# Optimization experiments

Hardware: AMD Instinct MI355X
Metric: run time of the kernel (lower is better)

## Reference

```python
import jax, jax.numpy as jnp
import numpy as np

N = 50000      # nodes
E = 400000     # edges (before self-loops)
IN = 128       # input feature dim
HID = 32       # out_channels per head
HEADS = 12
NC = 2         # num_classes
SLOPE = 0.2    # GATv2 leaky_relu negative slope


def setup_inputs() -> dict:
    key = jax.random.key(0)
    ks = jax.random.split(key, 24)
    f32 = jnp.float32
    def nrm(k, shape, s=0.1):
        return jax.random.normal(k, shape, dtype=f32) * s
    inp = {}
    inp["x"] = jax.random.normal(ks[0], (N, IN), dtype=f32)
    inp["edge_index"] = jax.random.randint(ks[1], (2, E), 0, N, dtype=jnp.int32)
    # GATv2 layer 0: in=IN, layer 1: in=HID; both heads=HEADS, out=HID, concat=False
    dims = [IN, HID]
    i = 2
    for l, d in enumerate(dims):
        inp[f"Wl{l}"] = nrm(ks[i], (d, HEADS * HID)); i += 1
        inp[f"bl{l}"] = jnp.zeros((HEADS * HID,), f32)
        inp[f"Wr{l}"] = nrm(ks[i], (d, HEADS * HID)); i += 1
        inp[f"br{l}"] = jnp.zeros((HEADS * HID,), f32)
        inp[f"att{l}"] = nrm(ks[i], (HEADS, HID)); i += 1
        inp[f"bias{l}"] = jnp.zeros((HID,), f32)
    # output GATv2Conv(HID, NC): heads=1, concat=True
    inp["Wlo"] = nrm(ks[i], (HID, NC)); i += 1
    inp["blo"] = jnp.zeros((NC,), f32)
    inp["Wro"] = nrm(ks[i], (HID, NC)); i += 1
    inp["bro"] = jnp.zeros((NC,), f32)
    inp["atto"] = nrm(ks[i], (1, NC)); i += 1
    inp["biaso"] = jnp.zeros((NC,), f32)
    return inp


def gatv2_conv(x, src, dst, Wl, bl, Wr, br, att, bias, heads, out_ch, concat):
    """PyG GATv2Conv (share_weights=False, self-loops pre-appended, eval mode)."""
    n = x.shape[0]
    xl = (x @ Wl + bl).reshape(n, heads, out_ch)   # source transform
    xr = (x @ Wr + br).reshape(n, heads, out_ch)   # target transform
    # per-edge attention: e_ij = att . leaky_relu(xl_j + xr_i)
    h = jax.nn.leaky_relu(xl[src] + xr[dst], SLOPE)            # [E, H, C]
    logits = jnp.einsum('ehc,hc->eh', h, att)                   # [E, H]
    # segment softmax over incoming edges per destination node
    m = jax.ops.segment_max(logits, dst, num_segments=n)        # [N, H]
    a = jnp.exp(logits - m[dst])
    denom = jax.ops.segment_sum(a, dst, num_segments=n)         # [N, H]
    alpha = a / (denom[dst] + 1e-16)                            # [E, H]
    out = jax.ops.segment_sum(xl[src] * alpha[..., None], dst, num_segments=n)
    out = out.reshape(n, heads * out_ch) if concat else out.mean(axis=1)
    return out + bias


def reference(x, edge_index, Wl0, bl0, Wr0, br0, att0, bias0,
              Wl1, bl1, Wr1, br1, att1, bias1,
              Wlo, blo, Wro, bro, atto, biaso):
    n = x.shape[0]
    loop = jnp.arange(n, dtype=edge_index.dtype)
    src = jnp.concatenate([edge_index[0], loop])  # add self-loops (PyG default)
    dst = jnp.concatenate([edge_index[1], loop])
    h = gatv2_conv(x, src, dst, Wl0, bl0, Wr0, br0, att0, bias0, HEADS, HID, False)
    h = jax.nn.elu(h)
    h = gatv2_conv(h, src, dst, Wl1, bl1, Wr1, br1, att1, bias1, HEADS, HID, False)
    h = jax.nn.elu(h)
    out = gatv2_conv(h, src, dst, Wlo, blo, Wro, bro, atto, biaso, 1, NC, True)
    return out
```

## Files before the change

kernel.cpp:

```cpp
#include <hip/hip_runtime.h>
#include <hip/hip_fp16.h>
#include <math.h>

#define IN_DIM 128
#define HID 32
#define HEADS 12
#define FDIM (HEADS*HID)
#define SLOPE 0.2f

typedef __attribute__((ext_vector_type(8))) short short8;
typedef __attribute__((ext_vector_type(4))) float float4v;
typedef __attribute__((ext_vector_type(4))) float f32x4;
typedef _Float16 hv2 __attribute__((ext_vector_type(2)));

__device__ __forceinline__ float dot2acc(hv2 a, hv2 b, float c) {
#if __has_builtin(__builtin_amdgcn_fdot2)
    return __builtin_amdgcn_fdot2(a, b, c, false);
#else
    return c + (float)a.x * (float)b.x + (float)a.y * (float)b.y;
#endif
}

__device__ __forceinline__ void async_cp16(const void* g, void* l) {
    __builtin_amdgcn_global_load_lds(
        (const __attribute__((address_space(1))) void*)g,
        (__attribute__((address_space(3))) void*)l, 16, 0, 0);
}


__global__ void hist_kernel(const int* __restrict__ dst, int* __restrict__ cnt, int E) {
    int e = blockIdx.x * blockDim.x + threadIdx.x;
    if (e < E) atomicAdd(&cnt[dst[e]], 1);
}

__global__ __launch_bounds__(256) void scan_partial_kernel(const int* __restrict__ cnt,
                                                           int* __restrict__ partials, int n) {
    int i = blockIdx.x * 256 + threadIdx.x;
    int v = (i < n) ? cnt[i] : 0;
#pragma unroll
    for (int off = 1; off < 64; off <<= 1) v += __shfl_xor(v, off);
    __shared__ int sh[4];
    if ((threadIdx.x & 63) == 0) sh[threadIdx.x >> 6] = v;
    __syncthreads();
    if (threadIdx.x == 0) partials[blockIdx.x] = sh[0] + sh[1] + sh[2] + sh[3];
}

__global__ __launch_bounds__(1024) void scan_top_kernel(int* __restrict__ partials, int nb) {
    __shared__ int sh[1024];
    int t = threadIdx.x;
    int v = (t < nb) ? partials[t] : 0;
    sh[t] = v;
    __syncthreads();
    for (int off = 1; off < 1024; off <<= 1) {
        int u = (t >= off) ? sh[t - off] : 0;
        __syncthreads();
        sh[t] += u;
        __syncthreads();
    }
    if (t < nb) partials[t] = sh[t] - v;
}

__global__ __launch_bounds__(256) void scan_final_kernel(const int* __restrict__ cnt,
                                                         const int* __restrict__ partials,
                                                         int* __restrict__ start,
                                                         int* __restrict__ cursor, int n) {
    __shared__ int sh[256];
    int t = threadIdx.x;
    int i = blockIdx.x * 256 + t;
    int v = (i < n) ? cnt[i] : 0;
    sh[t] = v;
    __syncthreads();
    for (int off = 1; off < 256; off <<= 1) {
        int u = (t >= off) ? sh[t - off] : 0;
        __syncthreads();
        sh[t] += u;
        __syncthreads();
    }
    int ex = sh[t] - v + partials[blockIdx.x];
    if (i < n) {
        start[i] = ex;
        cursor[i] = ex;
        if (i == n - 1) start[n] = ex + v;
    }
}

__global__ void scatter_kernel(const int* __restrict__ src, const int* __restrict__ dst,
                               int* __restrict__ cursor, int* __restrict__ srcs,
                               int* __restrict__ srcsOff, int E) {
    int e = blockIdx.x * blockDim.x + threadIdx.x;
    if (e < E) {
        int d = dst[e];
        int pos = atomicAdd(&cursor[d], 1);
        int s = src[e];
        srcs[pos] = s;
        srcsOff[pos] = s * (FDIM * 2);
    }
}


__device__ __forceinline__ unsigned int bf16_rne(float f) {
    unsigned int u = __float_as_uint(f);
    return (u + 0x7FFFu + ((u >> 16) & 1u)) >> 16;
}


__global__ void prep_all(const float* __restrict__ Wl0, const float* __restrict__ Wr0,
                         const float* __restrict__ Wl1, const float* __restrict__ Wr1,
                         const float* __restrict__ a0, const float* __restrict__ a1,
                         short* __restrict__ Bl0h, short* __restrict__ Bl0l,
                         short* __restrict__ Br0h, short* __restrict__ Br0l,
                         short* __restrict__ Bl1h, short* __restrict__ Bl1l,
                         short* __restrict__ Br1h, short* __restrict__ Br1l,
                         _Float16* __restrict__ attH) {
    int idx = blockIdx.x * 256 + threadIdx.x;
    if (idx < 49152) {
        int k = idx / 384, n = idx - k * 384;
        float w1 = Wl0[idx], w2 = Wr0[idx];
        unsigned int h1 = bf16_rne(w1);
        unsigned int l1 = bf16_rne(w1 - __uint_as_float(h1 << 16));
        unsigned int h2 = bf16_rne(w2);
        unsigned int l2 = bf16_rne(w2 - __uint_as_float(h2 << 16));
        Bl0h[n * 128 + k] = (short)h1;  Bl0l[n * 128 + k] = (short)l1;
        Br0h[n * 128 + k] = (short)h2;  Br0l[n * 128 + k] = (short)l2;
    } else if (idx < 61440) {
        int i2 = idx - 49152;
        int k = i2 / 384, n = i2 - k * 384;
        float w1 = Wl1[i2], w2 = Wr1[i2];
        unsigned int h1 = bf16_rne(w1);
        unsigned int l1 = bf16_rne(w1 - __uint_as_float(h1 << 16));
        unsigned int h2 = bf16_rne(w2);
        unsigned int l2 = bf16_rne(w2 - __uint_as_float(h2 << 16));
        Bl1h[n * 32 + k] = (short)h1;  Bl1l[n * 32 + k] = (short)l1;
        Br1h[n * 32 + k] = (short)h2;  Br1l[n * 32 + k] = (short)l2;
    } else if (idx < 62208) {
        int i2 = idx - 61440;
        attH[i2] = (_Float16)((i2 < 384) ? a0[i2] : a1[i2 - 384]);
    }
}


__global__ void conv_x_kernel(const float* __restrict__ A, short* __restrict__ Ah,
                              short* __restrict__ Al, int total4) {
    int i = blockIdx.x * 256 + threadIdx.x;
    if (i >= total4) return;
    float4 v = ((const float4*)A)[i];
    float fs[4] = {v.x, v.y, v.z, v.w};
    unsigned int hb[4], lb[4];
#pragma unroll
    for (int t = 0; t < 4; t++) {
        hb[t] = bf16_rne(fs[t]);
        lb[t] = bf16_rne(fs[t] - __uint_as_float(hb[t] << 16));
    }
    uint2 hp, lp;
    hp.x = hb[0] | (hb[1] << 16); hp.y = hb[2] | (hb[3] << 16);
    lp.x = lb[0] | (lb[1] << 16); lp.y = lb[2] | (lb[3] << 16);
    ((uint2*)Ah)[i] = hp;
    ((uint2*)Al)[i] = lp;
}


__global__ __launch_bounds__(256) void gemm_pair_async(
    const short* __restrict__ Ahi, const short* __restrict__ Alo,
    const short* __restrict__ B1h, const short* __restrict__ B1l,
    const float* __restrict__ bias1, __half* __restrict__ C1,
    const short* __restrict__ B2h, const short* __restrict__ B2l,
    const float* __restrict__ bias2, __half* __restrict__ C2,
    int M, int K) {
    __shared__ __align__(16) unsigned char smem[33792];
    int tid = threadIdx.x;
    int lane = tid & 63;
    int wave = tid >> 6;
    int wm = wave & 1, wn = wave >> 1;
    int rowBase = blockIdx.x * 128;
    bool second = blockIdx.y >= 3;
    int colBase = (blockIdx.y - (second ? 3 : 0)) * 128;
    const short* Bh  = second ? B2h : B1h;
    const short* Bl  = second ? B2l : B1l;
    const float* bias = second ? bias2 : bias1;
    __half*      C    = second ? C2 : C1;

    const short8* AsHi = (const short8*)smem;
    const short8* AsLo = (const short8*)(smem + 8192);
    const short8* BsHi = (const short8*)(smem + 16384);
    const short8* BsLo = (const short8*)(smem + 24576);

    const short* gsrc[8];
    void* ldst[8];
#pragma unroll
    for (int q = 0; q < 8; q++) {
        int t  = (q & 1) * 4 + wave;
        int rc = t * 16 + (lane & 15);
        int ko = (lane >> 4) * 8;
        const short* base = (q < 2) ? Ahi : (q < 4) ? Alo : (q < 6) ? Bh : Bl;
        int rb = (q < 4) ? rowBase : colBase;
        gsrc[q] = base + (long)(rb + rc) * K + ko;
        ldst[q] = (void*)(smem + q * 4096 + wave * 1024);
    }

    float4v acc[4][4];
#pragma unroll
    for (int i = 0; i < 4; i++)
#pragma unroll
        for (int j = 0; j < 4; j++) acc[i][j] = (float4v){0.f, 0.f, 0.f, 0.f};

    for (int kt = 0; kt < K; kt += 32) {
#pragma unroll
        for (int q = 0; q < 8; q++) {
            async_cp16(gsrc[q], ldst[q]);
            gsrc[q] += 32;
        }
        __syncthreads();

        short8 ah[4], al[4], bh[4], blv[4];
#pragma unroll
        for (int i = 0; i < 4; i++) {
            ah[i]  = AsHi[(wm * 4 + i) * 64 + lane];
            al[i]  = AsLo[(wm * 4 + i) * 64 + lane];
            bh[i]  = BsHi[(wn * 4 + i) * 64 + lane];
            blv[i] = BsLo[(wn * 4 + i) * 64 + lane];
        }
#pragma unroll
        for (int i = 0; i < 4; i++)
#pragma unroll
            for (int j = 0; j < 4; j++) {
                acc[i][j] = __builtin_amdgcn_mfma_f32_16x16x32_bf16(ah[i], bh[j],  acc[i][j], 0, 0, 0);
                acc[i][j] = __builtin_amdgcn_mfma_f32_16x16x32_bf16(ah[i], blv[j], acc[i][j], 0, 0, 0);
                acc[i][j] = __builtin_amdgcn_mfma_f32_16x16x32_bf16(al[i], bh[j],  acc[i][j], 0, 0, 0);
            }
        __syncthreads();
    }

    float* Ct = (float*)smem;
    int cq = lane >> 4, cn = lane & 15;
#pragma unroll
    for (int ph = 0; ph < 2; ph++) {
        if (wm == ph) {
#pragma unroll
            for (int i = 0; i < 4; i++)
#pragma unroll
                for (int j = 0; j < 4; j++) {
                    int lr = i * 16 + cq * 4;
                    int lc = wn * 64 + j * 16 + cn;
#pragma unroll
                    for (int r = 0; r < 4; r++)
                        Ct[(lr + r) * 132 + lc] = acc[i][j][r];
                }
        }
        __syncthreads();
#pragma unroll
        for (int k = 0; k < 4; k++) {
            int o = k * 256 + tid;
            int lr = o >> 4;
            int oc = (o & 15) << 3;
            int gr = rowBase + ph * 64 + lr;
            if (gr < M) {
                float4 f0 = *(float4*)&Ct[lr * 132 + oc];
                float4 f1 = *(float4*)&Ct[lr * 132 + oc + 4];
                int gc = colBase + oc;
                float4 b0 = *(const float4*)(bias + gc);
                float4 b1 = *(const float4*)(bias + gc + 4);
                __half2 p0 = __floats2half2_rn(f0.x + b0.x, f0.y + b0.y);
                __half2 p1 = __floats2half2_rn(f0.z + b0.z, f0.w + b0.w);
                __half2 p2 = __floats2half2_rn(f1.x + b1.x, f1.y + b1.y);
                __half2 p3 = __floats2half2_rn(f1.z + b1.z, f1.w + b1.w);
                uint4 ov;
                ov.x = *(unsigned int*)&p0;
                ov.y = *(unsigned int*)&p1;
                ov.z = *(unsigned int*)&p2;
                ov.w = *(unsigned int*)&p3;
                *(uint4*)(C + (size_t)gr * FDIM + gc) = ov;
            }
        }
        __syncthreads();
    }
}


__global__ __launch_bounds__(64) void agg_kernel(const __half* __restrict__ xl,
                                                 const __half* __restrict__ xr,
                                                 const _Float16* __restrict__ att_h,
                                                 const float* __restrict__ bias,
                                                 const int* __restrict__ start,
                                                 const int* __restrict__ srcsOff,
                                                 short* __restrict__ houtHi,
                                                 short* __restrict__ houtLo,
                                                 const float* __restrict__ Wl,
                                                 const float* __restrict__ bl,
                                                 const float* __restrict__ Wr,
                                                 const float* __restrict__ br,
                                                 float* __restrict__ xloB,
                                                 float* __restrict__ xroB, int N) {
    int node = blockIdx.x;
    if (node >= N) return;
    int lane = threadIdx.x & 63;
    int hl = lane & 31;
    int half_ = lane >> 5;
    int cb = hl << 3;

    long nodeOff = (long)node * (FDIM * 2);
    hv2 xr2[6], at2[6];
    f32x4 acc[3];
    float s[3];
#pragma unroll
    for (int c = 0; c < 3; c++) {
        uint2 ur = *(const uint2*)((const char*)xr + nodeOff + c * 256 + cb);
        xr2[2*c]   = __builtin_bit_cast(hv2, ur.x);
        xr2[2*c+1] = __builtin_bit_cast(hv2, ur.y);
        uint2 ua = *(const uint2*)((const char*)att_h + c * 256 + cb);
        at2[2*c]   = __builtin_bit_cast(hv2, ua.x);
        at2[2*c+1] = __builtin_bit_cast(hv2, ua.y);
        acc[c] = (f32x4){0.f, 0.f, 0.f, 0.f};
        s[c] = 0.f;
    }
    const hv2 sl2 = {(_Float16)SLOPE, (_Float16)SLOPE};
    const char* xlb = (const char*)xl;

    int e0 = start[node], e1 = start[node + 1];

    for (int b = e0 - 1; b < e1; b += 4) {
        hv2 xa[2][6];
        float mask[2];
#pragma unroll
        for (int p = 0; p < 2; p++) {
            int myIdx = b + p * 2 + half_;
            int ic = min(myIdx, e1 - 1);
            long off = (ic < e0) ? nodeOff : (long)srcsOff[ic];
            mask[p] = (myIdx < e1) ? 0.f : -1e30f;
            const char* base = xlb + off + cb;
            uint2 u0 = *(const uint2*)(base);
            uint2 u1 = *(const uint2*)(base + 256);
            uint2 u2 = *(const uint2*)(base + 512);
            xa[p][0] = __builtin_bit_cast(hv2, u0.x); xa[p][1] = __builtin_bit_cast(hv2, u0.y);
            xa[p][2] = __builtin_bit_cast(hv2, u1.x); xa[p][3] = __builtin_bit_cast(hv2, u1.y);
            xa[p][4] = __builtin_bit_cast(hv2, u2.x); xa[p][5] = __builtin_bit_cast(hv2, u2.y);
        }
#pragma unroll
        for (int p = 0; p < 2; p++) {
            float pc[3];
#pragma unroll
            for (int c = 0; c < 3; c++) {
                hv2 t0 = xa[p][2*c]   + xr2[2*c];
                hv2 t1 = xa[p][2*c+1] + xr2[2*c+1];
                t0 = __builtin_elementwise_max(t0, t0 * sl2);
                t1 = __builtin_elementwise_max(t1, t1 * sl2);
                pc[c] = dot2acc(t1, at2[2*c+1], dot2acc(t0, at2[2*c], 0.f));
            }
#pragma unroll
            for (int st = 1; st <= 4; st <<= 1) {
                pc[0] += __shfl_xor(pc[0], st);
                pc[1] += __shfl_xor(pc[1], st);
                pc[2] += __shfl_xor(pc[2], st);
            }
#pragma unroll
            for (int c = 0; c < 3; c++) {
                float a = __expf(pc[c] + mask[p]);
                s[c] += a;
                acc[c].x = fmaf(a, (float)xa[p][2*c].x,   acc[c].x);
                acc[c].y = fmaf(a, (float)xa[p][2*c].y,   acc[c].y);
                acc[c].z = fmaf(a, (float)xa[p][2*c+1].x, acc[c].z);
                acc[c].w = fmaf(a, (float)xa[p][2*c+1].y, acc[c].w);
            }
        }
    }

#pragma unroll
    for (int c = 0; c < 3; c++) {
        acc[c].x += __shfl_xor(acc[c].x, 32);
        acc[c].y += __shfl_xor(acc[c].y, 32);
        acc[c].z += __shfl_xor(acc[c].z, 32);
        acc[c].w += __shfl_xor(acc[c].w, 32);
        s[c] += __shfl_xor(s[c], 32);
    }
    f32x4 v[3];
#pragma unroll
    for (int c = 0; c < 3; c++) {
        float inv = 1.f / (s[c] + 1e-16f);
        f32x4 iv = {inv, inv, inv, inv};
        v[c] = acc[c] * iv;
    }
#pragma unroll
    for (int st = 8; st <= 16; st <<= 1) {
#pragma unroll
        for (int c = 0; c < 3; c++) {
            v[c].x += __shfl_xor(v[c].x, st);
            v[c].y += __shfl_xor(v[c].y, st);
            v[c].z += __shfl_xor(v[c].z, st);
            v[c].w += __shfl_xor(v[c].w, st);
        }
    }
    if (lane < 8) {
        f32x4 b4 = *(const f32x4*)(bias + (hl << 2));
        f32x4 o = (v[0] + v[1] + v[2]) * (f32x4){1.f/12.f, 1.f/12.f, 1.f/12.f, 1.f/12.f} + b4;
        o.x = o.x > 0.f ? o.x : expm1f(o.x);
        o.y = o.y > 0.f ? o.y : expm1f(o.y);
        o.z = o.z > 0.f ? o.z : expm1f(o.z);
        o.w = o.w > 0.f ? o.w : expm1f(o.w);
        if (houtHi) {
            float fs[4] = {o.x, o.y, o.z, o.w};
            unsigned int hb[4], lb[4];
#pragma unroll
            for (int t = 0; t < 4; t++) {
                hb[t] = bf16_rne(fs[t]);
                lb[t] = bf16_rne(fs[t] - __uint_as_float(hb[t] << 16));
            }
            uint2 hp, lp;
            hp.x = hb[0] | (hb[1] << 16); hp.y = hb[2] | (hb[3] << 16);
            lp.x = lb[0] | (lb[1] << 16); lp.y = lb[2] | (lb[3] << 16);
            *(uint2*)(houtHi + (size_t)node * 32 + (hl << 2)) = hp;
            *(uint2*)(houtLo + (size_t)node * 32 + (hl << 2)) = lp;
        }
        if (Wl) {
            f32x4 wl0 = *(const f32x4*)(Wl + (hl << 3));
            f32x4 wl1 = *(const f32x4*)(Wl + (hl << 3) + 4);
            f32x4 wr0 = *(const f32x4*)(Wr + (hl << 3));
            f32x4 wr1 = *(const f32x4*)(Wr + (hl << 3) + 4);
            float l0 = o.x * wl0.x + o.y * wl0.z + o.z * wl1.x + o.w * wl1.z;
            float l1 = o.x * wl0.y + o.y * wl0.w + o.z * wl1.y + o.w * wl1.w;
            float r0 = o.x * wr0.x + o.y * wr0.z + o.z * wr1.x + o.w * wr1.z;
            float r1 = o.x * wr0.y + o.y * wr0.w + o.z * wr1.y + o.w * wr1.w;
#pragma unroll
            for (int st = 1; st <= 4; st <<= 1) {
                l0 += __shfl_xor(l0, st); l1 += __shfl_xor(l1, st);
                r0 += __shfl_xor(r0, st); r1 += __shfl_xor(r1, st);
            }
            if (hl == 0) {
                xloB[2 * node]     = l0 + bl[0];
                xloB[2 * node + 1] = l1 + bl[1];
                xroB[2 * node]     = r0 + br[0];
                xroB[2 * node + 1] = r1 + br[1];
            }
        }
    }
}


__global__ __launch_bounds__(256) void out_agg_kernel(const float* __restrict__ xlo,
                                                      const float* __restrict__ xro,
                                                      const float* __restrict__ atto,
                                                      const float* __restrict__ biaso,
                                                      const int* __restrict__ start,
                                                      const int* __restrict__ srcs,
                                                      float* __restrict__ out, int N) {
    int g = (blockIdx.x * blockDim.x + threadIdx.x) >> 3;
    int j = threadIdx.x & 7;
    if (g >= N) return;
    float a0 = atto[0], a1 = atto[1];
    float xr0 = xro[2 * g], xr1 = xro[2 * g + 1];
    float s = 0.f, acc0 = 0.f, acc1 = 0.f;
    int e0 = start[g], e1 = start[g + 1];
    for (int idx = e0 - 1 + j; idx < e1; idx += 8) {
        int jj = (idx < e0) ? g : srcs[idx];
        float x0 = xlo[2 * jj], x1 = xlo[2 * jj + 1];
        float t0 = x0 + xr0, t1 = x1 + xr1;
        t0 = fmaxf(t0, SLOPE * t0);
        t1 = fmaxf(t1, SLOPE * t1);
        float L = a0 * t0 + a1 * t1;
        float a = __expf(L);
        s += a;
        acc0 = fmaf(a, x0, acc0);
        acc1 = fmaf(a, x1, acc1);
    }
#pragma unroll
    for (int st = 1; st <= 4; st <<= 1) {
        s    += __shfl_xor(s, st);
        acc0 += __shfl_xor(acc0, st);
        acc1 += __shfl_xor(acc1, st);
    }
    if (j == 0) {
        float inv = 1.0f / (s + 1e-16f);
        out[2 * g]     = acc0 * inv + biaso[0];
        out[2 * g + 1] = acc1 * inv + biaso[1];
    }
}


extern "C" void kernel_launch(void* const* d_in, const int* in_sizes, int n_in,
                              void* d_out, int out_size, void* d_ws, size_t ws_size,
                              hipStream_t stream) {
    const float* x    = (const float*)d_in[0];
    const int*   ei   = (const int*)d_in[1];
    const float* Wl0  = (const float*)d_in[2];
    const float* bl0  = (const float*)d_in[3];
    const float* Wr0  = (const float*)d_in[4];
    const float* br0  = (const float*)d_in[5];
    const float* att0 = (const float*)d_in[6];
    const float* bias0= (const float*)d_in[7];
    const float* Wl1  = (const float*)d_in[8];
    const float* bl1  = (const float*)d_in[9];
    const float* Wr1  = (const float*)d_in[10];
    const float* br1  = (const float*)d_in[11];
    const float* att1 = (const float*)d_in[12];
    const float* bias1= (const float*)d_in[13];
    const float* Wlo  = (const float*)d_in[14];
    const float* blo  = (const float*)d_in[15];
    const float* Wro  = (const float*)d_in[16];
    const float* bro  = (const float*)d_in[17];
    const float* atto = (const float*)d_in[18];
    const float* biaso= (const float*)d_in[19];

    const int N = in_sizes[0] / IN_DIM;
    const int E = in_sizes[1] / 2;

    char* ws = (char*)d_ws;
    size_t off = 0;
    auto take = [&](size_t bytes) -> char* {
        char* p = ws + off;
        off += (bytes + 255) & ~(size_t)255;
        return p;
    };
    __half* xlf = (__half*)take((size_t)N * FDIM * 2);
    __half* xrf = (__half*)take((size_t)N * FDIM * 2);
    float* xloB = (float*)take((size_t)N * 2 * 4);
    float* xroB = (float*)take((size_t)N * 2 * 4);
    int* cnt    = (int*)take((size_t)N * 4);
    int* startA = (int*)take((size_t)(N + 1) * 4);
    int* cursor = (int*)take((size_t)N * 4);
    int* srcs   = (int*)take((size_t)E * 4);
    int* srcsOff= (int*)take((size_t)E * 4);
    int  nb     = (N + 255) / 256;
    int* partials = (int*)take((size_t)nb * 4);
    short* Bl0h = (short*)take((size_t)FDIM * IN_DIM * 2);
    short* Bl0l = (short*)take((size_t)FDIM * IN_DIM * 2);
    short* Br0h = (short*)take((size_t)FDIM * IN_DIM * 2);
    short* Br0l = (short*)take((size_t)FDIM * IN_DIM * 2);
    short* Bl1h = (short*)take((size_t)FDIM * HID * 2);
    short* Bl1l = (short*)take((size_t)FDIM * HID * 2);
    short* Br1h = (short*)take((size_t)FDIM * HID * 2);
    short* Br1l = (short*)take((size_t)FDIM * HID * 2);
    short* xh   = (short*)take((size_t)N * IN_DIM * 2);
    short* xlo_ = (short*)take((size_t)N * IN_DIM * 2);
    short* h0h  = (short*)take((size_t)N * HID * 2);
    short* h0l  = (short*)take((size_t)N * HID * 2);
    _Float16* attH = (_Float16*)take((size_t)768 * 2);
    (void)take(32768);

    const int* esrc = ei;
    const int* edst = ei + E;

    prep_all<<<(62208 + 255) / 256, 256, 0, stream>>>(Wl0, Wr0, Wl1, Wr1, att0, att1,
                                                      Bl0h, Bl0l, Br0h, Br0l,
                                                      Bl1h, Bl1l, Br1h, Br1l, attH);
    conv_x_kernel<<<((N * IN_DIM / 4) + 255) / 256, 256, 0, stream>>>(x, xh, xlo_, N * IN_DIM / 4);

    hipMemsetAsync(cnt, 0, (size_t)N * 4, stream);
    hist_kernel<<<(E + 255) / 256, 256, 0, stream>>>(edst, cnt, E);
    scan_partial_kernel<<<nb, 256, 0, stream>>>(cnt, partials, N);
    scan_top_kernel<<<1, 1024, 0, stream>>>(partials, nb);
    scan_final_kernel<<<nb, 256, 0, stream>>>(cnt, partials, startA, cursor, N);
    scatter_kernel<<<(E + 255) / 256, 256, 0, stream>>>(esrc, edst, cursor, srcs, srcsOff, E);

    dim3 ggrid((N + 127) / 128, 6);
    gemm_pair_async<<<ggrid, 256, 0, stream>>>(xh, xlo_, Bl0h, Bl0l, bl0, xlf, Br0h, Br0l, br0, xrf, N, IN_DIM);
    agg_kernel<<<N, 64, 0, stream>>>(xlf, xrf, attH, bias0, startA, srcsOff,
                                     h0h, h0l, nullptr, nullptr, nullptr, nullptr,
                                     nullptr, nullptr, N);
    gemm_pair_async<<<ggrid, 256, 0, stream>>>(h0h, h0l, Bl1h, Bl1l, bl1, xlf, Br1h, Br1l, br1, xrf, N, HID);
    agg_kernel<<<N, 64, 0, stream>>>(xlf, xrf, attH + 384, bias1, startA, srcsOff,
                                     nullptr, nullptr, Wlo, blo, Wro, bro,
                                     xloB, xroB, N);
    out_agg_kernel<<<((size_t)N * 8 + 255) / 256, 256, 0, stream>>>(xloB, xroB, atto, biaso, startA, srcs, (float*)d_out, N);
}
```

Baseline: 382.5 us.

## Remap GATv2 aggregation so each lane owns one head of one edge

The aggregation kernel changes its work split. Before, 32 lanes covered one edge's 384 features and used shuffle reductions for the per-head dot products. Now each of 60 lanes handles one head (32 channels) of one of 5 edges at a time, so the attention logit is computed within a lane with no shuffles. Partial sums are combined across the 5 edge slots through a per-wave LDS buffer with a rotated layout to avoid bank conflicts. Blocks now hold 4 waves, each processing its own node. The trade-off is far more registers per lane (16 accumulator vectors plus xr/att copies), which may lower occupancy, and 4 lanes per wave sit idle.

```diff
diff --git a/kernel.cpp b/kernel.cpp
--- a/kernel.cpp
+++ b/kernel.cpp
@@ -276,159 +276,158 @@
 }
 
 
-__global__ __launch_bounds__(64) void agg_kernel(const __half* __restrict__ xl,
-                                                 const __half* __restrict__ xr,
-                                                 const _Float16* __restrict__ att_h,
-                                                 const float* __restrict__ bias,
-                                                 const int* __restrict__ start,
-                                                 const int* __restrict__ srcsOff,
-                                                 short* __restrict__ houtHi,
-                                                 short* __restrict__ houtLo,
-                                                 const float* __restrict__ Wl,
-                                                 const float* __restrict__ bl,
-                                                 const float* __restrict__ Wr,
-                                                 const float* __restrict__ br,
-                                                 float* __restrict__ xloB,
-                                                 float* __restrict__ xroB, int N) {
-    int node = blockIdx.x;
+__global__ __launch_bounds__(256) void agg_kernel(const __half* __restrict__ xl,
+                                                  const __half* __restrict__ xr,
+                                                  const _Float16* __restrict__ att_h,
+                                                  const float* __restrict__ bias,
+                                                  const int* __restrict__ start,
+                                                  const int* __restrict__ srcsOff,
+                                                  short* __restrict__ houtHi,
+                                                  short* __restrict__ houtLo,
+                                                  const float* __restrict__ Wl,
+                                                  const float* __restrict__ bl,
+                                                  const float* __restrict__ Wr,
+                                                  const float* __restrict__ br,
+                                                  float* __restrict__ xloB,
+                                                  float* __restrict__ xroB, int N) {
+    __shared__ float lds[4][2048];
+    int wave = threadIdx.x >> 6;
+    int lane = threadIdx.x & 63;
+    int node = blockIdx.x * 4 + wave;
     if (node >= N) return;
-    int lane = threadIdx.x & 63;
-    int hl = lane & 31;
-    int half_ = lane >> 5;
-    int cb = hl << 3;
+    float* W = lds[wave];
+
+    int h = lane % 12;
+    int slot = (lane < 60) ? (lane / 12) : (1 << 28);
 
     long nodeOff = (long)node * (FDIM * 2);
-    hv2 xr2[6], at2[6];
-    f32x4 acc[3];
-    float s[3];
-#pragma unroll
-    for (int c = 0; c < 3; c++) {
-        uint2 ur = *(const uint2*)((const char*)xr + nodeOff + c * 256 + cb);
-        xr2[2*c]   = __builtin_bit_cast(hv2, ur.x);
-        xr2[2*c+1] = __builtin_bit_cast(hv2, ur.y);
-        uint2 ua = *(const uint2*)((const char*)att_h + c * 256 + cb);
-        at2[2*c]   = __builtin_bit_cast(hv2, ua.x);
-        at2[2*c+1] = __builtin_bit_cast(hv2, ua.y);
-        acc[c] = (f32x4){0.f, 0.f, 0.f, 0.f};
-        s[c] = 0.f;
+    int hb = h << 6;
+
+    hv2 xr2[16], at2[16];
+    {
+        const uint4* xrp = (const uint4*)((const char*)xr + nodeOff + hb);
+        const uint4* atp = (const uint4*)((const char*)att_h + hb);
+#pragma unroll
+        for (int q = 0; q < 4; q++) {
+            uint4 u = xrp[q];
+            xr2[q * 4 + 0] = __builtin_bit_cast(hv2, u.x);
+            xr2[q * 4 + 1] = __builtin_bit_cast(hv2, u.y);
+            xr2[q * 4 + 2] = __builtin_bit_cast(hv2, u.z);
+            xr2[q * 4 + 3] = __builtin_bit_cast(hv2, u.w);
+            uint4 v = atp[q];
+            at2[q * 4 + 0] = __builtin_bit_cast(hv2, v.x);
+            at2[q * 4 + 1] = __builtin_bit_cast(hv2, v.y);
+            at2[q * 4 + 2] = __builtin_bit_cast(hv2, v.z);
+            at2[q * 4 + 3] = __builtin_bit_cast(hv2, v.w);
+        }
     }
     const hv2 sl2 = {(_Float16)SLOPE, (_Float16)SLOPE};
     const char* xlb = (const char*)xl;
 
     int e0 = start[node], e1 = start[node + 1];
 
-    for (int b = e0 - 1; b < e1; b += 4) {
-        hv2 xa[2][6];
-        float mask[2];
-#pragma unroll
-        for (int p = 0; p < 2; p++) {
-            int myIdx = b + p * 2 + half_;
-            int ic = min(myIdx, e1 - 1);
-            long off = (ic < e0) ? nodeOff : (long)srcsOff[ic];
-            mask[p] = (myIdx < e1) ? 0.f : -1e30f;
-            const char* base = xlb + off + cb;
-            uint2 u0 = *(const uint2*)(base);
-            uint2 u1 = *(const uint2*)(base + 256);
-            uint2 u2 = *(const uint2*)(base + 512);
-            xa[p][0] = __builtin_bit_cast(hv2, u0.x); xa[p][1] = __builtin_bit_cast(hv2, u0.y);
-            xa[p][2] = __builtin_bit_cast(hv2, u1.x); xa[p][3] = __builtin_bit_cast(hv2, u1.y);
-            xa[p][4] = __builtin_bit_cast(hv2, u2.x); xa[p][5] = __builtin_bit_cast(hv2, u2.y);
-        }
-#pragma unroll
-        for (int p = 0; p < 2; p++) {
-            float pc[3];
-#pragma unroll
-            for (int c = 0; c < 3; c++) {
-                hv2 t0 = xa[p][2*c]   + xr2[2*c];
-                hv2 t1 = xa[p][2*c+1] + xr2[2*c+1];
-                t0 = __builtin_elementwise_max(t0, t0 * sl2);
-                t1 = __builtin_elementwise_max(t1, t1 * sl2);
-                pc[c] = dot2acc(t1, at2[2*c+1], dot2acc(t0, at2[2*c], 0.f));
+    float s = 0.f;
+    f32x4 acc[8];
+#pragma unroll
+    for (int q = 0; q < 8; q++) acc[q] = (f32x4){0.f, 0.f, 0.f, 0.f};
+
+    for (int base = e0 - 1; base < e1; base += 5) {
+        int myIdx = base + slot;
+        int ic = min(myIdx, e1 - 1);
+        long off = (ic < e0) ? nodeOff : (long)srcsOff[ic];
+        float mask = (myIdx < e1) ? 0.f : -1e30f;
+        const uint4* p = (const uint4*)(xlb + off + hb);
+        uint4 u0 = p[0], u1 = p[1], u2 = p[2], u3 = p[3];
+        hv2 xa[16];
+        xa[0]  = __builtin_bit_cast(hv2, u0.x); xa[1]  = __builtin_bit_cast(hv2, u0.y);
+        xa[2]  = __builtin_bit_cast(hv2, u0.z); xa[3]  = __builtin_bit_cast(hv2, u0.w);
+        xa[4]  = __builtin_bit_cast(hv2, u1.x); xa[5]  = __builtin_bit_cast(hv2, u1.y);
+        xa[6]  = __builtin_bit_cast(hv2, u1.z); xa[7]  = __builtin_bit_cast(hv2, u1.w);
+        xa[8]  = __builtin_bit_cast(hv2, u2.x); xa[9]  = __builtin_bit_cast(hv2, u2.y);
+        xa[10] = __builtin_bit_cast(hv2, u2.z); xa[11] = __builtin_bit_cast(hv2, u2.w);
+        xa[12] = __builtin_bit_cast(hv2, u3.x); xa[13] = __builtin_bit_cast(hv2, u3.y);
+        xa[14] = __builtin_bit_cast(hv2, u3.z); xa[15] = __builtin_bit_cast(hv2, u3.w);
+
+        float pc0 = 0.f, pc1 = 0.f;
+#pragma unroll
+        for (int k = 0; k < 16; k += 2) {
+            hv2 t0 = xa[k] + xr2[k];
+            hv2 t1 = xa[k + 1] + xr2[k + 1];
+            t0 = __builtin_elementwise_max(t0, t0 * sl2);
+            t1 = __builtin_elementwise_max(t1, t1 * sl2);
+            pc0 = dot2acc(t0, at2[k], pc0);
+            pc1 = dot2acc(t1, at2[k + 1], pc1);
+        }
+        float a = __expf(pc0 + pc1 + mask);
+        s += a;
+#pragma unroll
+        for (int k = 0; k < 16; k++) {
+            if (k & 1) {
+                acc[k >> 1].z = fmaf(a, (float)xa[k].x, acc[k >> 1].z);
+                acc[k >> 1].w = fmaf(a, (float)xa[k].y, acc[k >> 1].w);
+            } else {
+                acc[k >> 1].x = fmaf(a, (float)xa[k].x, acc[k >> 1].x);
+                acc[k >> 1].y = fmaf(a, (float)xa[k].y, acc[k >> 1].y);
             }
-#pragma unroll
-            for (int st = 1; st <= 4; st <<= 1) {
-                pc[0] += __shfl_xor(pc[0], st);
-                pc[1] += __shfl_xor(pc[1], st);
-                pc[2] += __shfl_xor(pc[2], st);
-            }
-#pragma unroll
-            for (int c = 0; c < 3; c++) {
-                float a = __expf(pc[c] + mask[p]);
-                s[c] += a;
-                acc[c].x = fmaf(a, (float)xa[p][2*c].x,   acc[c].x);
-                acc[c].y = fmaf(a, (float)xa[p][2*c].y,   acc[c].y);
-                acc[c].z = fmaf(a, (float)xa[p][2*c+1].x, acc[c].z);
-                acc[c].w = fmaf(a, (float)xa[p][2*c+1].y, acc[c].w);
-            }
-        }
-    }
-
-#pragma unroll
-    for (int c = 0; c < 3; c++) {
-        acc[c].x += __shfl_xor(acc[c].x, 32);
-        acc[c].y += __shfl_xor(acc[c].y, 32);
-        acc[c].z += __shfl_xor(acc[c].z, 32);
-        acc[c].w += __shfl_xor(acc[c].w, 32);
-        s[c] += __shfl_xor(s[c], 32);
-    }
-    f32x4 v[3];
-#pragma unroll
-    for (int c = 0; c < 3; c++) {
-        float inv = 1.f / (s[c] + 1e-16f);
-        f32x4 iv = {inv, inv, inv, inv};
-        v[c] = acc[c] * iv;
-    }
-#pragma unroll
-    for (int st = 8; st <= 16; st <<= 1) {
-#pragma unroll
-        for (int c = 0; c < 3; c++) {
-            v[c].x += __shfl_xor(v[c].x, st);
-            v[c].y += __shfl_xor(v[c].y, st);
-            v[c].z += __shfl_xor(v[c].z, st);
-            v[c].w += __shfl_xor(v[c].w, st);
-        }
-    }
-    if (lane < 8) {
-        f32x4 b4 = *(const f32x4*)(bias + (hl << 2));
-        f32x4 o = (v[0] + v[1] + v[2]) * (f32x4){1.f/12.f, 1.f/12.f, 1.f/12.f, 1.f/12.f} + b4;
-        o.x = o.x > 0.f ? o.x : expm1f(o.x);
-        o.y = o.y > 0.f ? o.y : expm1f(o.y);
-        o.z = o.z > 0.f ? o.z : expm1f(o.z);
-        o.w = o.w > 0.f ? o.w : expm1f(o.w);
-        if (houtHi) {
-            float fs[4] = {o.x, o.y, o.z, o.w};
-            unsigned int hb[4], lb[4];
-#pragma unroll
-            for (int t = 0; t < 4; t++) {
-                hb[t] = bf16_rne(fs[t]);
-                lb[t] = bf16_rne(fs[t] - __uint_as_float(hb[t] << 16));
-            }
-            uint2 hp, lp;
-            hp.x = hb[0] | (hb[1] << 16); hp.y = hb[2] | (hb[3] << 16);
-            lp.x = lb[0] | (lb[1] << 16); lp.y = lb[2] | (lb[3] << 16);
-            *(uint2*)(houtHi + (size_t)node * 32 + (hl << 2)) = hp;
-            *(uint2*)(houtLo + (size_t)node * 32 + (hl << 2)) = lp;
-        }
-        if (Wl) {
-            f32x4 wl0 = *(const f32x4*)(Wl + (hl << 3));
-            f32x4 wl1 = *(const f32x4*)(Wl + (hl << 3) + 4);
-            f32x4 wr0 = *(const f32x4*)(Wr + (hl << 3));
-            f32x4 wr1 = *(const f32x4*)(Wr + (hl << 3) + 4);
-            float l0 = o.x * wl0.x + o.y * wl0.z + o.z * wl1.x + o.w * wl1.z;
-            float l1 = o.x * wl0.y + o.y * wl0.w + o.z * wl1.y + o.w * wl1.w;
-            float r0 = o.x * wr0.x + o.y * wr0.z + o.z * wr1.x + o.w * wr1.z;
-            float r1 = o.x * wr0.y + o.y * wr0.w + o.z * wr1.y + o.w * wr1.w;
-#pragma unroll
-            for (int st = 1; st <= 4; st <<= 1) {
-                l0 += __shfl_xor(l0, st); l1 += __shfl_xor(l1, st);
-                r0 += __shfl_xor(r0, st); r1 += __shfl_xor(r1, st);
-            }
-            if (hl == 0) {
-                xloB[2 * node]     = l0 + bl[0];
-                xloB[2 * node + 1] = l1 + bl[1];
-                xroB[2 * node]     = r0 + br[0];
-                xroB[2 * node + 1] = r1 + br[1];
-            }
+        }
+    }
+
+    if (lane < 60) {
+#pragma unroll
+        for (int q = 0; q < 8; q++)
+            *(f32x4*)&W[lane * 32 + (((q + lane) & 7) << 2)] = acc[q];
+        W[1920 + lane] = s;
+    }
+    asm volatile("s_waitcnt lgkmcnt(0)" ::: "memory");
+    if (lane < 12) {
+        float sv = W[1920 + lane] + W[1932 + lane] + W[1944 + lane] +
+                   W[1956 + lane] + W[1968 + lane];
+        W[1980 + lane] = 1.f / (sv + 1e-16f);
+    }
+    asm volatile("s_waitcnt lgkmcnt(0)" ::: "memory");
+
+    int c = lane & 31;
+    int g = lane >> 5;
+    float o = 0.f;
+#pragma unroll
+    for (int hh = 0; hh < 6; hh++) {
+        int hd = g * 6 + hh;
+        float inv = W[1980 + hd];
+        float t = 0.f;
+#pragma unroll
+        for (int s5 = 0; s5 < 5; s5++) {
+            int r = hd + 12 * s5;
+            t += W[r * 32 + ((((c >> 2) + r) & 7) << 2) + (c & 3)];
+        }
+        o = fmaf(inv, t, o);
+    }
+    o += __shfl_xor(o, 32);
+    o = o * (1.f / 12.f) + bias[c];
+    o = o > 0.f ? o : expm1f(o);
+
+    if (houtHi) {
+        unsigned int hbi = bf16_rne(o);
+        unsigned int lbi = bf16_rne(o - __uint_as_float(hbi << 16));
+        if (lane < 32) {
+            houtHi[(size_t)node * 32 + c] = (short)hbi;
+            houtLo[(size_t)node * 32 + c] = (short)lbi;
+        }
+    }
+    if (Wl) {
+        float2 wl = *(const float2*)(Wl + 2 * c);
+        float2 wr = *(const float2*)(Wr + 2 * c);
+        float l0 = o * wl.x, l1 = o * wl.y;
+        float r0 = o * wr.x, r1 = o * wr.y;
+#pragma unroll
+        for (int st = 1; st <= 16; st <<= 1) {
+            l0 += __shfl_xor(l0, st); l1 += __shfl_xor(l1, st);
+            r0 += __shfl_xor(r0, st); r1 += __shfl_xor(r1, st);
+        }
+        if (lane == 0) {
+            xloB[2 * node]     = l0 + bl[0];
+            xloB[2 * node + 1] = l1 + bl[1];
+            xroB[2 * node]     = r0 + br[0];
+            xroB[2 * node + 1] = r1 + br[1];
         }
     }
 }
@@ -550,13 +549,14 @@
     scatter_kernel<<<(E + 255) / 256, 256, 0, stream>>>(esrc, edst, cursor, srcs, srcsOff, E);
 
     dim3 ggrid((N + 127) / 128, 6);
+    int aggGrid = (N + 3) / 4;
     gemm_pair_async<<<ggrid, 256, 0, stream>>>(xh, xlo_, Bl0h, Bl0l, bl0, xlf, Br0h, Br0l, br0, xrf, N, IN_DIM);
-    agg_kernel<<<N, 64, 0, stream>>>(xlf, xrf, attH, bias0, startA, srcsOff,
-                                     h0h, h0l, nullptr, nullptr, nullptr, nullptr,
-                                     nullptr, nullptr, N);
+    agg_kernel<<<aggGrid, 256, 0, stream>>>(xlf, xrf, attH, bias0, startA, srcsOff,
+                                            h0h, h0l, nullptr, nullptr, nullptr, nullptr,
+                                            nullptr, nullptr, N);
     gemm_pair_async<<<ggrid, 256, 0, stream>>>(h0h, h0l, Bl1h, Bl1l, bl1, xlf, Br1h, Br1l, br1, xrf, N, HID);
-    agg_kernel<<<N, 64, 0, stream>>>(xlf, xrf, attH + 384, bias1, startA, srcsOff,
-                                     nullptr, nullptr, Wlo, blo, Wro, bro,
-                                     xloB, xroB, N);
+    agg_kernel<<<aggGrid, 256, 0, stream>>>(xlf, xrf, attH + 384, bias1, startA, srcsOff,
+                                            nullptr, nullptr, Wlo, blo, Wro, bro,
+                                            xloB, xroB, N);
     out_agg_kernel<<<((size_t)N * 8 + 255) / 256, 256, 0, stream>>>(xloB, xroB, atto, biaso, startA, srcs, (float*)d_out, N);
 }
```

New measurement: 419.0 us. +9.5%, slower.

## Software-pipeline edge gathers in GAT aggregation and pack four nodes per block

Applied to the files above, without the earlier changes.

Restructures the aggregation loop into a double-buffered pipeline: neighbor offsets are prefetched two steps ahead and feature gathers one step ahead of the softmax/accumulate compute, to hide gather latency. Blocks now hold four wavefronts (one node each) with launch bounds of 256 threads and a min-blocks hint, cutting the grid size fourfold. Offsets switch to 32-bit ints. The extra live registers for two gather buffers raise register pressure, and the last step issues loads for out-of-range indices that get clamped.

```diff
diff --git a/kernel.cpp b/kernel.cpp
--- a/kernel.cpp
+++ b/kernel.cpp
@@ -276,34 +276,34 @@
 }
 
 
-__global__ __launch_bounds__(64) void agg_kernel(const __half* __restrict__ xl,
-                                                 const __half* __restrict__ xr,
-                                                 const _Float16* __restrict__ att_h,
-                                                 const float* __restrict__ bias,
-                                                 const int* __restrict__ start,
-                                                 const int* __restrict__ srcsOff,
-                                                 short* __restrict__ houtHi,
-                                                 short* __restrict__ houtLo,
-                                                 const float* __restrict__ Wl,
-                                                 const float* __restrict__ bl,
-                                                 const float* __restrict__ Wr,
-                                                 const float* __restrict__ br,
-                                                 float* __restrict__ xloB,
-                                                 float* __restrict__ xroB, int N) {
-    int node = blockIdx.x;
+__global__ __launch_bounds__(256, 8) void agg_kernel(const __half* __restrict__ xl,
+                                                     const __half* __restrict__ xr,
+                                                     const _Float16* __restrict__ att_h,
+                                                     const float* __restrict__ bias,
+                                                     const int* __restrict__ start,
+                                                     const int* __restrict__ srcsOff,
+                                                     short* __restrict__ houtHi,
+                                                     short* __restrict__ houtLo,
+                                                     const float* __restrict__ Wl,
+                                                     const float* __restrict__ bl,
+                                                     const float* __restrict__ Wr,
+                                                     const float* __restrict__ br,
+                                                     float* __restrict__ xloB,
+                                                     float* __restrict__ xroB, int N) {
+    int lane = threadIdx.x & 63;
+    int node = blockIdx.x * 4 + (threadIdx.x >> 6);
     if (node >= N) return;
-    int lane = threadIdx.x & 63;
     int hl = lane & 31;
     int half_ = lane >> 5;
     int cb = hl << 3;
 
-    long nodeOff = (long)node * (FDIM * 2);
+    int nodeOffI = node * (FDIM * 2);
     hv2 xr2[6], at2[6];
     f32x4 acc[3];
     float s[3];
 #pragma unroll
     for (int c = 0; c < 3; c++) {
-        uint2 ur = *(const uint2*)((const char*)xr + nodeOff + c * 256 + cb);
+        uint2 ur = *(const uint2*)((const char*)xr + nodeOffI + c * 256 + cb);
         xr2[2*c]   = __builtin_bit_cast(hv2, ur.x);
         xr2[2*c+1] = __builtin_bit_cast(hv2, ur.y);
         uint2 ua = *(const uint2*)((const char*)att_h + c * 256 + cb);
@@ -313,29 +313,37 @@
         s[c] = 0.f;
     }
     const hv2 sl2 = {(_Float16)SLOPE, (_Float16)SLOPE};
-    const char* xlb = (const char*)xl;
+    const char* xlb = (const char*)xl + cb;
 
     int e0 = start[node], e1 = start[node + 1];
-
-    for (int b = e0 - 1; b < e1; b += 4) {
-        hv2 xa[2][6];
-        float mask[2];
+    int e1m1 = e1 - 1;
+
+    auto prepOff = [&](int b, int (&off)[2]) {
 #pragma unroll
         for (int p = 0; p < 2; p++) {
             int myIdx = b + p * 2 + half_;
-            int ic = min(myIdx, e1 - 1);
-            long off = (ic < e0) ? nodeOff : (long)srcsOff[ic];
-            mask[p] = (myIdx < e1) ? 0.f : -1e30f;
-            const char* base = xlb + off + cb;
-            uint2 u0 = *(const uint2*)(base);
-            uint2 u1 = *(const uint2*)(base + 256);
-            uint2 u2 = *(const uint2*)(base + 512);
+            int ic = min(myIdx, e1m1);
+            int so = srcsOff[ic];
+            off[p] = (ic < e0) ? nodeOffI : so;
+        }
+    };
+    auto gather = [&](const int (&off)[2], hv2 (&xa)[2][6]) {
+#pragma unroll
+        for (int p = 0; p < 2; p++) {
+            const char* b = xlb + off[p];
+            uint2 u0 = *(const uint2*)(b);
+            uint2 u1 = *(const uint2*)(b + 256);
+            uint2 u2 = *(const uint2*)(b + 512);
             xa[p][0] = __builtin_bit_cast(hv2, u0.x); xa[p][1] = __builtin_bit_cast(hv2, u0.y);
             xa[p][2] = __builtin_bit_cast(hv2, u1.x); xa[p][3] = __builtin_bit_cast(hv2, u1.y);
             xa[p][4] = __builtin_bit_cast(hv2, u2.x); xa[p][5] = __builtin_bit_cast(hv2, u2.y);
         }
+    };
+    auto compute = [&](int b, const hv2 (&xa)[2][6]) {
 #pragma unroll
         for (int p = 0; p < 2; p++) {
+            int myIdx = b + p * 2 + half_;
+            float mask = (myIdx < e1) ? 0.f : -1e30f;
             float pc[3];
 #pragma unroll
             for (int c = 0; c < 3; c++) {
@@ -353,7 +361,7 @@
             }
 #pragma unroll
             for (int c = 0; c < 3; c++) {
-                float a = __expf(pc[c] + mask[p]);
+                float a = __expf(pc[c] + mask);
                 s[c] += a;
                 acc[c].x = fmaf(a, (float)xa[p][2*c].x,   acc[c].x);
                 acc[c].y = fmaf(a, (float)xa[p][2*c].y,   acc[c].y);
@@ -361,6 +369,27 @@
                 acc[c].w = fmaf(a, (float)xa[p][2*c+1].y, acc[c].w);
             }
         }
+    };
+
+    int offA[2], offB[2];
+    hv2 xaA[2][6], xaB[2][6];
+    int base = e0 - 1;
+    prepOff(base, offA);
+    gather(offA, xaA);
+    prepOff(base + 4, offB);
+
+    while (true) {
+        gather(offB, xaB);
+        prepOff(base + 8, offA);
+        compute(base, xaA);
+        base += 4;
+        if (base >= e1) break;
+
+        gather(offA, xaA);
+        prepOff(base + 8, offB);
+        compute(base, xaB);
+        base += 4;
+        if (base >= e1) break;
     }
 
 #pragma unroll
@@ -550,13 +579,14 @@
     scatter_kernel<<<(E + 255) / 256, 256, 0, stream>>>(esrc, edst, cursor, srcs, srcsOff, E);
 
     dim3 ggrid((N + 127) / 128, 6);
+    int aggGrid = (N + 3) / 4;
     gemm_pair_async<<<ggrid, 256, 0, stream>>>(xh, xlo_, Bl0h, Bl0l, bl0, xlf, Br0h, Br0l, br0, xrf, N, IN_DIM);
-    agg_kernel<<<N, 64, 0, stream>>>(xlf, xrf, attH, bias0, startA, srcsOff,
-                                     h0h, h0l, nullptr, nullptr, nullptr, nullptr,
-                                     nullptr, nullptr, N);
+    agg_kernel<<<aggGrid, 256, 0, stream>>>(xlf, xrf, attH, bias0, startA, srcsOff,
+                                            h0h, h0l, nullptr, nullptr, nullptr, nullptr,
+                                            nullptr, nullptr, N);
     gemm_pair_async<<<ggrid, 256, 0, stream>>>(h0h, h0l, Bl1h, Bl1l, bl1, xlf, Br1h, Br1l, br1, xrf, N, HID);
-    agg_kernel<<<N, 64, 0, stream>>>(xlf, xrf, attH + 384, bias1, startA, srcsOff,
-                                     nullptr, nullptr, Wlo, blo, Wro, bro,
-                                     xloB, xroB, N);
+    agg_kernel<<<aggGrid, 256, 0, stream>>>(xlf, xrf, attH + 384, bias1, startA, srcsOff,
+                                            nullptr, nullptr, Wlo, blo, Wro, bro,
+                                            xloB, xroB, N);
     out_agg_kernel<<<((size_t)N * 8 + 255) / 256, 256, 0, stream>>>(xloB, xroB, atto, biaso, startA, srcs, (float*)d_out, N);
 }
```

Result: slower. 738.3 us (+93.0%).

## Store self-loops in CSR, split mask-free main loop, fold log2e into attention

Applied to the files above, without the earlier changes.

Self-loop edges are now written into the CSR edge list by a new kernel, so the aggregation loops no longer need a per-edge branch for the implicit self edge. The main aggregation loop handles full groups of four edges without masking, and a separate masked tail handles the remainder. Attention vectors are pre-scaled by log2(e) so the softmax can use the hardware exp2 directly, and inline v_fma_mix instructions fuse the fp16-to-fp32 conversion into the accumulate FMAs. This adds one small launch, N extra CSR entries, and some code duplication.

```diff
diff --git a/kernel.cpp b/kernel.cpp
--- a/kernel.cpp
+++ b/kernel.cpp
@@ -7,6 +7,7 @@
 #define HEADS 12
 #define FDIM (HEADS*HID)
 #define SLOPE 0.2f
+#define LOG2E 1.44269504f
 
 typedef __attribute__((ext_vector_type(8))) short short8;
 typedef __attribute__((ext_vector_type(4))) float float4v;
@@ -21,6 +22,27 @@
 #endif
 }
 
+__device__ __forceinline__ float exp2h(float x) {
+#if __has_builtin(__builtin_amdgcn_exp2f)
+    return __builtin_amdgcn_exp2f(x);
+#else
+    return exp2f(x);
+#endif
+}
+
+__device__ __forceinline__ float fma_mix_lo(hv2 x, float a, float c) {
+    float d;
+    asm("v_fma_mix_f32 %0, %1, %2, %3 op_sel_hi:[1,0,0]"
+        : "=v"(d) : "v"(x), "v"(a), "v"(c));
+    return d;
+}
+__device__ __forceinline__ float fma_mix_hi(hv2 x, float a, float c) {
+    float d;
+    asm("v_fma_mix_f32 %0, %1, %2, %3 op_sel:[1,0,0] op_sel_hi:[1,0,0]"
+        : "=v"(d) : "v"(x), "v"(a), "v"(c));
+    return d;
+}
+
 __device__ __forceinline__ void async_cp16(const void* g, void* l) {
     __builtin_amdgcn_global_load_lds(
         (const __attribute__((address_space(1))) void*)g,
@@ -36,7 +58,7 @@
 __global__ __launch_bounds__(256) void scan_partial_kernel(const int* __restrict__ cnt,
                                                            int* __restrict__ partials, int n) {
     int i = blockIdx.x * 256 + threadIdx.x;
-    int v = (i < n) ? cnt[i] : 0;
+    int v = (i < n) ? cnt[i] + 1 : 0;
 #pragma unroll
     for (int off = 1; off < 64; off <<= 1) v += __shfl_xor(v, off);
     __shared__ int sh[4];
@@ -67,7 +89,7 @@
     __shared__ int sh[256];
     int t = threadIdx.x;
     int i = blockIdx.x * 256 + t;
-    int v = (i < n) ? cnt[i] : 0;
+    int v = (i < n) ? cnt[i] + 1 : 0;
     sh[t] = v;
     __syncthreads();
     for (int off = 1; off < 256; off <<= 1) {
@@ -94,6 +116,16 @@
         int s = src[e];
         srcs[pos] = s;
         srcsOff[pos] = s * (FDIM * 2);
+    }
+}
+
+__global__ void selfloop_kernel(const int* __restrict__ cursor, int* __restrict__ srcs,
+                                int* __restrict__ srcsOff, int N) {
+    int i = blockIdx.x * 256 + threadIdx.x;
+    if (i < N) {
+        int p = cursor[i];
+        srcs[p] = i;
+        srcsOff[p] = i * (FDIM * 2);
     }
 }
 
@@ -134,7 +166,7 @@
         Br1h[n * 32 + k] = (short)h2;  Br1l[n * 32 + k] = (short)l2;
     } else if (idx < 62208) {
         int i2 = idx - 61440;
-        attH[i2] = (_Float16)((i2 < 384) ? a0[i2] : a1[i2 - 384]);
+        attH[i2] = (_Float16)(((i2 < 384) ? a0[i2] : a1[i2 - 384]) * LOG2E);
     }
 }
 
@@ -313,20 +345,16 @@
         s[c] = 0.f;
     }
     const hv2 sl2 = {(_Float16)SLOPE, (_Float16)SLOPE};
-    const char* xlb = (const char*)xl;
+    const char* xlb = (const char*)xl + cb;
 
     int e0 = start[node], e1 = start[node + 1];
-
-    for (int b = e0 - 1; b < e1; b += 4) {
+    int b = e0;
+
+    for (; b + 4 <= e1; b += 4) {
         hv2 xa[2][6];
-        float mask[2];
 #pragma unroll
         for (int p = 0; p < 2; p++) {
-            int myIdx = b + p * 2 + half_;
-            int ic = min(myIdx, e1 - 1);
-            long off = (ic < e0) ? nodeOff : (long)srcsOff[ic];
-            mask[p] = (myIdx < e1) ? 0.f : -1e30f;
-            const char* base = xlb + off + cb;
+            const char* base = xlb + (long)srcsOff[b + p * 2 + half_];
             uint2 u0 = *(const uint2*)(base);
             uint2 u1 = *(const uint2*)(base + 256);
             uint2 u2 = *(const uint2*)(base + 512);
@@ -353,12 +381,57 @@
             }
 #pragma unroll
             for (int c = 0; c < 3; c++) {
-                float a = __expf(pc[c] + mask[p]);
+                float a = exp2h(pc[c]);
                 s[c] += a;
-                acc[c].x = fmaf(a, (float)xa[p][2*c].x,   acc[c].x);
-                acc[c].y = fmaf(a, (float)xa[p][2*c].y,   acc[c].y);
-                acc[c].z = fmaf(a, (float)xa[p][2*c+1].x, acc[c].z);
-                acc[c].w = fmaf(a, (float)xa[p][2*c+1].y, acc[c].w);
+                acc[c].x = fma_mix_lo(xa[p][2*c],   a, acc[c].x);
+                acc[c].y = fma_mix_hi(xa[p][2*c],   a, acc[c].y);
+                acc[c].z = fma_mix_lo(xa[p][2*c+1], a, acc[c].z);
+                acc[c].w = fma_mix_hi(xa[p][2*c+1], a, acc[c].w);
+            }
+        }
+    }
+
+    if (b < e1) {
+        hv2 xa[2][6];
+        float mask[2];
+#pragma unroll
+        for (int p = 0; p < 2; p++) {
+            int myIdx = b + p * 2 + half_;
+            int ic = min(myIdx, e1 - 1);
+            mask[p] = (myIdx < e1) ? 0.f : -1e30f;
+            const char* base = xlb + (long)srcsOff[ic];
+            uint2 u0 = *(const uint2*)(base);
+            uint2 u1 = *(const uint2*)(base + 256);
+            uint2 u2 = *(const uint2*)(base + 512);
+            xa[p][0] = __builtin_bit_cast(hv2, u0.x); xa[p][1] = __builtin_bit_cast(hv2, u0.y);
+            xa[p][2] = __builtin_bit_cast(hv2, u1.x); xa[p][3] = __builtin_bit_cast(hv2, u1.y);
+            xa[p][4] = __builtin_bit_cast(hv2, u2.x); xa[p][5] = __builtin_bit_cast(hv2, u2.y);
+        }
+#pragma unroll
+        for (int p = 0; p < 2; p++) {
+            float pc[3];
+#pragma unroll
+            for (int c = 0; c < 3; c++) {
+                hv2 t0 = xa[p][2*c]   + xr2[2*c];
+                hv2 t1 = xa[p][2*c+1] + xr2[2*c+1];
+                t0 = __builtin_elementwise_max(t0, t0 * sl2);
+                t1 = __builtin_elementwise_max(t1, t1 * sl2);
+                pc[c] = dot2acc(t1, at2[2*c+1], dot2acc(t0, at2[2*c], 0.f));
+            }
+#pragma unroll
+            for (int st = 1; st <= 4; st <<= 1) {
+                pc[0] += __shfl_xor(pc[0], st);
+                pc[1] += __shfl_xor(pc[1], st);
+                pc[2] += __shfl_xor(pc[2], st);
+            }
+#pragma unroll
+            for (int c = 0; c < 3; c++) {
+                float a = exp2h(pc[c] + mask[p]);
+                s[c] += a;
+                acc[c].x = fma_mix_lo(xa[p][2*c],   a, acc[c].x);
+                acc[c].y = fma_mix_hi(xa[p][2*c],   a, acc[c].y);
+                acc[c].z = fma_mix_lo(xa[p][2*c+1], a, acc[c].z);
+                acc[c].w = fma_mix_hi(xa[p][2*c+1], a, acc[c].w);
             }
         }
     }
@@ -444,18 +517,17 @@
     int g = (blockIdx.x * blockDim.x + threadIdx.x) >> 3;
     int j = threadIdx.x & 7;
     if (g >= N) return;
-    float a0 = atto[0], a1 = atto[1];
+    float a0 = atto[0] * LOG2E, a1 = atto[1] * LOG2E;
     float xr0 = xro[2 * g], xr1 = xro[2 * g + 1];
     float s = 0.f, acc0 = 0.f, acc1 = 0.f;
     int e0 = start[g], e1 = start[g + 1];
-    for (int idx = e0 - 1 + j; idx < e1; idx += 8) {
-        int jj = (idx < e0) ? g : srcs[idx];
+    for (int idx = e0 + j; idx < e1; idx += 8) {
+        int jj = srcs[idx];
         float x0 = xlo[2 * jj], x1 = xlo[2 * jj + 1];
         float t0 = x0 + xr0, t1 = x1 + xr1;
         t0 = fmaxf(t0, SLOPE * t0);
         t1 = fmaxf(t1, SLOPE * t1);
-        float L = a0 * t0 + a1 * t1;
-        float a = __expf(L);
+        float a = exp2h(a0 * t0 + a1 * t1);
         s += a;
         acc0 = fmaf(a, x0, acc0);
         acc1 = fmaf(a, x1, acc1);
@@ -515,8 +587,8 @@
     int* cnt    = (int*)take((size_t)N * 4);
     int* startA = (int*)take((size_t)(N + 1) * 4);
     int* cursor = (int*)take((size_t)N * 4);
-    int* srcs   = (int*)take((size_t)E * 4);
-    int* srcsOff= (int*)take((size_t)E * 4);
+    int* srcs   = (int*)take((size_t)(E + N) * 4);
+    int* srcsOff= (int*)take((size_t)(E + N) * 4);
     int  nb     = (N + 255) / 256;
     int* partials = (int*)take((size_t)nb * 4);
     short* Bl0h = (short*)take((size_t)FDIM * IN_DIM * 2);
@@ -548,6 +620,7 @@
     scan_top_kernel<<<1, 1024, 0, stream>>>(partials, nb);
     scan_final_kernel<<<nb, 256, 0, stream>>>(cnt, partials, startA, cursor, N);
     scatter_kernel<<<(E + 255) / 256, 256, 0, stream>>>(esrc, edst, cursor, srcs, srcsOff, E);
+    selfloop_kernel<<<nb, 256, 0, stream>>>(cursor, srcs, srcsOff, N);
 
     dim3 ggrid((N + 127) / 128, 6);
     gemm_pair_async<<<ggrid, 256, 0, stream>>>(xh, xlo_, Bl0h, Bl0l, bl0, xlf, Br0h, Br0l, br0, xrf, N, IN_DIM);
```

Result: no change. 377.5 us (-1.3%).
